# Performance work log

Measured on AMD Instinct MI355X. Metric: run time of the kernel, lower is better.

## Reference

```python
import jax, jax.numpy as jnp
import numpy as np

HIDDEN_DIM = 64
MEMORY_SLOTS = 8
SEQ_LEN = 64
VOCAB_SIZE = 64
B = 524288


def setup_inputs() -> dict:
    key = jax.random.key(0)
    k1, k2, k3, k4, k5, k6 = jax.random.split(key, 6)
    seqs = jax.random.randint(k1, (B, SEQ_LEN), 0, VOCAB_SIZE + 2, dtype=jnp.int64 if jax.config.jax_enable_x64 else jnp.int32)
    query_tok = jax.random.randint(k2, (B,), 0, VOCAB_SIZE + 2, dtype=seqs.dtype)
    embed = jax.random.normal(k3, (VOCAB_SIZE + 2, HIDDEN_DIM), dtype=jnp.float32)
    # torch Linear: y = x @ W.T + b
    W1 = jax.random.normal(k4, (HIDDEN_DIM, HIDDEN_DIM * 2), dtype=jnp.float32) * (1.0 / np.sqrt(HIDDEN_DIM * 2))
    b1 = jnp.zeros((HIDDEN_DIM,), dtype=jnp.float32)
    W2 = jax.random.normal(k5, (VOCAB_SIZE, HIDDEN_DIM), dtype=jnp.float32) * (1.0 / np.sqrt(HIDDEN_DIM))
    b2 = jnp.zeros((VOCAB_SIZE,), dtype=jnp.float32)
    return {"seqs": seqs, "query_tok": query_tok, "embed": embed,
            "W1": W1, "b1": b1, "W2": W2, "b2": b2}


def reference(seqs, query_tok, embed, W1, b1, W2, b2):
    # FIFO of capacity MEMORY_SLOTS over tokens t=0..SEQ_LEN-2 keeps exactly the
    # last MEMORY_SLOTS tokens: positions [SEQ_LEN-1-MEMORY_SLOTS, SEQ_LEN-1).
    win = seqs[:, SEQ_LEN - 1 - MEMORY_SLOTS : SEQ_LEN - 1]        # [B, 8]
    mem_summary = embed[win].mean(axis=1)                          # [B, H]
    q_emb = embed[query_tok]                                       # [B, H]
    h = jnp.concatenate([q_emb, mem_summary], axis=-1)             # [B, 2H]
    h = jax.nn.relu(h @ W1.T + b1)                                 # [B, H]
    logits = h @ W2.T + b2                                         # [B, VOCAB]
    return logits
```

## Files before the change

kernel.cpp:

```cpp
#include <hip/hip_runtime.h>

#define HID 64
#define NTOK 66
#define SEQ 64
#define WIN0 55
#define NW 8
#define LDS_STRIDE 72
#define ITERS 8
#define BLOCK 512
#define ROWS_PER_ITER 128
#define HOFF (2 * NTOK * LDS_STRIDE)
#define HBUF (ROWS_PER_ITER * LDS_STRIDE)

typedef _Float16 half8 __attribute__((ext_vector_type(8)));
typedef unsigned short ushort8v __attribute__((ext_vector_type(8)));
typedef float float4v __attribute__((ext_vector_type(4)));

static __device__ __forceinline__ unsigned short f2h(float f) {
    _Float16 h = (_Float16)f;
    union { _Float16 h; unsigned short u; } v; v.h = h;
    return v.u;
}

__global__ void build_tables(const float* __restrict__ embed,
                             const float* __restrict__ W1,
                             const float* __restrict__ b1,
                             unsigned short* __restrict__ tbl) {
    int b = blockIdx.x;
    int tb = b & 1;
    int t  = b >> 1;
    int n  = threadIdx.x;
    float acc = tb ? 0.0f : b1[n];
    const float* er = embed + t * HID;
    const float* wr = W1 + n * (2 * HID) + tb * HID;
#pragma unroll 8
    for (int k = 0; k < HID; ++k) acc += er[k] * wr[k];
    if (tb) acc *= 0.125f;
    tbl[tb * (NTOK * HID) + t * HID + n] = f2h(acc);
}

__global__ __launch_bounds__(BLOCK, 2) void fused_forward(
    const int* __restrict__ seqs,
    const int* __restrict__ qtok,
    const float* __restrict__ W2,
    const float* __restrict__ b2,
    const unsigned short* __restrict__ tbl,
    float* __restrict__ out)
{
    __shared__ unsigned short T_lds[HOFF + 2 * HBUF];

    int tid  = threadIdx.x;
    int wv   = tid >> 6;
    int l    = tid & 63;
    int lrow = l & 15;
    int lg   = l >> 4;
    int lk8  = lg * 8;
    int tile0 = wv & 3;

    int blk0 = blockIdx.x * (ITERS * ROWS_PER_ITER);
    int prow0 = blk0 + tile0 * 16 + lrow;
    int prow1 = prow0 + 64;

    int qA0, qA1, qB0, qB1;
    int wA0[NW], wA1[NW], wB0[NW], wB1[NW];

#define LOADT(S, t_) if ((t_) < ITERS) { \
    int r0_ = prow0 + (t_) * ROWS_PER_ITER; \
    int r1_ = prow1 + (t_) * ROWS_PER_ITER; \
    q##S##0 = qtok[r0_]; \
    q##S##1 = qtok[r1_]; \
    const int* s0_ = seqs + r0_ * SEQ + WIN0; \
    const int* s1_ = seqs + r1_ * SEQ + WIN0; \
    _Pragma("unroll") \
    for (int j = 0; j < NW; ++j) { w##S##0[j] = s0_[j]; w##S##1[j] = s1_[j]; } \
}

#define RD_T1(qq, koff) (*(const half8*)(T_lds + (qq) * LDS_STRIDE + (koff)))
#define RD_T2(ww, koff) (*(const half8*)(T_lds + NTOK * LDS_STRIDE + (ww) * LDS_STRIDE + (koff)))

#define PRODUCE(S, buf_) { \
    unsigned short* hb_ = T_lds + HOFF + (buf_) * HBUF; \
    half8 s0_ = RD_T1(q##S##0, lk8); \
    half8 s1_ = RD_T1(q##S##0, 32 + lk8); \
    half8 u0_ = RD_T1(q##S##1, lk8); \
    half8 u1_ = RD_T1(q##S##1, 32 + lk8); \
    _Pragma("unroll") \
    for (int j = 0; j < NW; ++j) { \
        s0_ += RD_T2(w##S##0[j], lk8); \
        s1_ += RD_T2(w##S##0[j], 32 + lk8); \
        u0_ += RD_T2(w##S##1[j], lk8); \
        u1_ += RD_T2(w##S##1[j], 32 + lk8); \
    } \
    half8 z_ = (half8)(_Float16)0; \
    s0_ = __builtin_elementwise_max(s0_, z_); \
    s1_ = __builtin_elementwise_max(s1_, z_); \
    u0_ = __builtin_elementwise_max(u0_, z_); \
    u1_ = __builtin_elementwise_max(u1_, z_); \
    unsigned short* r0_ = hb_ + (tile0 * 16 + lrow) * LDS_STRIDE; \
    unsigned short* r1_ = hb_ + ((tile0 + 4) * 16 + lrow) * LDS_STRIDE; \
    *(half8*)(r0_ + lk8) = s0_; \
    *(half8*)(r0_ + 32 + lk8) = s1_; \
    *(half8*)(r1_ + lk8) = u0_; \
    *(half8*)(r1_ + 32 + lk8) = u1_; \
}

#define CONSUME(t_, buf_) { \
    const unsigned short* hb_ = T_lds + HOFF + (buf_) * HBUF; \
    _Pragma("unroll") \
    for (int pt = 0; pt < 2; ++pt) { \
        int trow_ = (tile0 + pt * 4) * 16 + lrow; \
        half8 a0_ = *(const half8*)(hb_ + trow_ * LDS_STRIDE + lk8); \
        half8 a1_ = *(const half8*)(hb_ + trow_ * LDS_STRIDE + 32 + lk8); \
        float* op_ = out + (size_t)(blk0 + (t_) * ROWS_PER_ITER + trow_) * HID; \
        _Pragma("unroll") \
        for (int nt = 0; nt < 4; ++nt) { \
            float4v acc_ = __builtin_amdgcn_mfma_f32_16x16x32_f16(wfrag[nt][0], a0_, b2v[nt], 0, 0, 0); \
            acc_ = __builtin_amdgcn_mfma_f32_16x16x32_f16(wfrag[nt][1], a1_, acc_, 0, 0, 0); \
            *(float4v*)(op_ + nt * 16 + lg * 4) = acc_; \
        } \
    } \
}

#define ITER_E(t_) { \
    if (wv >= 4) { CONSUME(t_, (t_) & 1); } \
    else if ((t_) + 1 < ITERS) { PRODUCE(B, ((t_) + 1) & 1); LOADT(B, (t_) + 3); } \
    __syncthreads(); \
}
#define ITER_O(t_) { \
    if (wv >= 4) { CONSUME(t_, (t_) & 1); } \
    else if ((t_) + 1 < ITERS) { PRODUCE(A, ((t_) + 1) & 1); LOADT(A, (t_) + 3); } \
    __syncthreads(); \
}

    half8   wfrag[4][2];
    float4v b2v[4];
    if (wv < 4) {
        LOADT(A, 0);
        LOADT(B, 1);
    } else {
#pragma unroll
        for (int nt = 0; nt < 4; ++nt) {
            b2v[nt] = *(const float4v*)(b2 + nt * 16 + lg * 4);
#pragma unroll
            for (int kc = 0; kc < 2; ++kc) {
                const float* wp = W2 + (nt * 16 + lrow) * HID + kc * 32 + lk8;
                half8 f;
#pragma unroll
                for (int j = 0; j < 8; ++j) f[j] = (_Float16)wp[j];
                wfrag[nt][kc] = f;
            }
        }
    }

    for (int i = tid; i < 2 * NTOK * (HID / 8); i += BLOCK) {
        int tbi = i / (NTOK * 8);
        int rem = i - tbi * (NTOK * 8);
        int t   = rem >> 3;
        int kq  = (rem & 7) << 3;
        *(ushort8v*)(T_lds + tbi * (NTOK * LDS_STRIDE) + t * LDS_STRIDE + kq) =
            *(const ushort8v*)(tbl + tbi * (NTOK * HID) + t * HID + kq);
    }
    __syncthreads();

    if (wv < 4) {
        PRODUCE(A, 0);
        LOADT(A, 2);
    }
    __syncthreads();

    ITER_E(0);  ITER_O(1);  ITER_E(2);  ITER_O(3);
    ITER_E(4);  ITER_O(5);  ITER_E(6);  ITER_O(7);

#undef LOADT
#undef RD_T1
#undef RD_T2
#undef PRODUCE
#undef CONSUME
#undef ITER_E
#undef ITER_O
}

extern "C" void kernel_launch(void* const* d_in, const int* in_sizes, int n_in,
                              void* d_out, int out_size, void* d_ws, size_t ws_size,
                              hipStream_t stream) {
    const int*   seqs  = (const int*)d_in[0];
    const int*   qtok  = (const int*)d_in[1];
    const float* embed = (const float*)d_in[2];
    const float* W1    = (const float*)d_in[3];
    const float* b1    = (const float*)d_in[4];
    const float* W2    = (const float*)d_in[5];
    const float* b2    = (const float*)d_in[6];
    float* out = (float*)d_out;
    unsigned short* tbl = (unsigned short*)d_ws;

    int B = in_sizes[0] / SEQ;

    build_tables<<<NTOK * 2, HID, 0, stream>>>(embed, W1, b1, tbl);

    int grid = B / (ITERS * ROWS_PER_ITER);
    fused_forward<<<grid, BLOCK, 0, stream>>>(seqs, qtok, W2, b2, tbl, out);
}
```

Measured before the change: 46.40 us.

## Process two row-tiles per barrier with four-deep LDS ring and more rows per block

Doubles rows per block (ITERS 8 to 16) and restructures the producer/consumer pipeline so each barrier round produces and consumes two 128-row tiles, using four H buffers in LDS and four sets of prefetched token registers. The aim is to halve the number of __syncthreads per row and to deepen global prefetch so the index loads are further ahead of use. In exchange it uses more LDS and registers (four q/w register sets), which may lower occupancy, and the grid is halved.

```diff
diff --git a/kernel.cpp b/kernel.cpp
--- a/kernel.cpp
+++ b/kernel.cpp
@@ -6,7 +6,7 @@
 #define WIN0 55
 #define NW 8
 #define LDS_STRIDE 72
-#define ITERS 8
+#define ITERS 16
 #define BLOCK 512
 #define ROWS_PER_ITER 128
 #define HOFF (2 * NTOK * LDS_STRIDE)
@@ -47,7 +47,7 @@
     const unsigned short* __restrict__ tbl,
     float* __restrict__ out)
 {
-    __shared__ unsigned short T_lds[HOFF + 2 * HBUF];
+    __shared__ unsigned short T_lds[HOFF + 4 * HBUF];
 
     int tid  = threadIdx.x;
     int wv   = tid >> 6;
@@ -61,35 +61,38 @@
     int prow0 = blk0 + tile0 * 16 + lrow;
     int prow1 = prow0 + 64;
 
-    int qA0, qA1, qB0, qB1;
-    int wA0[NW], wA1[NW], wB0[NW], wB1[NW];
-
-#define LOADT(S, t_) if ((t_) < ITERS) { \
+    int qS0, qS1, qS2, qS3;
+    int wS0[NW], wS1[NW], wS2[NW], wS3[NW];
+
+#define LOADT(S, t_) { \
     int r0_ = prow0 + (t_) * ROWS_PER_ITER; \
     int r1_ = prow1 + (t_) * ROWS_PER_ITER; \
-    q##S##0 = qtok[r0_]; \
-    q##S##1 = qtok[r1_]; \
+    qS##S = qtok[r0_]; \
+     \
+    q2S##S = qtok[r1_]; \
     const int* s0_ = seqs + r0_ * SEQ + WIN0; \
     const int* s1_ = seqs + r1_ * SEQ + WIN0; \
     _Pragma("unroll") \
-    for (int j = 0; j < NW; ++j) { w##S##0[j] = s0_[j]; w##S##1[j] = s1_[j]; } \
-}
+    for (int j = 0; j < NW; ++j) { wS##S[j] = s0_[j]; w2S##S[j] = s1_[j]; } \
+}
+    int q2S0, q2S1, q2S2, q2S3;
+    int w2S0[NW], w2S1[NW], w2S2[NW], w2S3[NW];
 
 #define RD_T1(qq, koff) (*(const half8*)(T_lds + (qq) * LDS_STRIDE + (koff)))
 #define RD_T2(ww, koff) (*(const half8*)(T_lds + NTOK * LDS_STRIDE + (ww) * LDS_STRIDE + (koff)))
 
 #define PRODUCE(S, buf_) { \
     unsigned short* hb_ = T_lds + HOFF + (buf_) * HBUF; \
-    half8 s0_ = RD_T1(q##S##0, lk8); \
-    half8 s1_ = RD_T1(q##S##0, 32 + lk8); \
-    half8 u0_ = RD_T1(q##S##1, lk8); \
-    half8 u1_ = RD_T1(q##S##1, 32 + lk8); \
+    half8 s0_ = RD_T1(qS##S, lk8); \
+    half8 s1_ = RD_T1(qS##S, 32 + lk8); \
+    half8 u0_ = RD_T1(q2S##S, lk8); \
+    half8 u1_ = RD_T1(q2S##S, 32 + lk8); \
     _Pragma("unroll") \
     for (int j = 0; j < NW; ++j) { \
-        s0_ += RD_T2(w##S##0[j], lk8); \
-        s1_ += RD_T2(w##S##0[j], 32 + lk8); \
-        u0_ += RD_T2(w##S##1[j], lk8); \
-        u1_ += RD_T2(w##S##1[j], 32 + lk8); \
+        s0_ += RD_T2(wS##S[j], lk8); \
+        s1_ += RD_T2(wS##S[j], 32 + lk8); \
+        u0_ += RD_T2(w2S##S[j], lk8); \
+        u1_ += RD_T2(w2S##S[j], 32 + lk8); \
     } \
     half8 z_ = (half8)(_Float16)0; \
     s0_ = __builtin_elementwise_max(s0_, z_); \
@@ -121,22 +124,23 @@
     } \
 }
 
-#define ITER_E(t_) { \
-    if (wv >= 4) { CONSUME(t_, (t_) & 1); } \
-    else if ((t_) + 1 < ITERS) { PRODUCE(B, ((t_) + 1) & 1); LOADT(B, (t_) + 3); } \
-    __syncthreads(); \
-}
-#define ITER_O(t_) { \
-    if (wv >= 4) { CONSUME(t_, (t_) & 1); } \
-    else if ((t_) + 1 < ITERS) { PRODUCE(A, ((t_) + 1) & 1); LOADT(A, (t_) + 3); } \
+#define ROUND(i0, i1, l0, l1, doload) { \
+    if (wv >= 4) { CONSUME(i0, (i0) & 3); CONSUME(i1, (i1) & 3); } \
+    else { \
+        PRODUCE(((i0 + 2) & 3), ((i0 + 2) & 3)); \
+        PRODUCE(((i1 + 2) & 3), ((i1 + 2) & 3)); \
+        if (doload) { LOADT(((l0) & 3), l0); LOADT(((l1) & 3), l1); } \
+    } \
     __syncthreads(); \
 }
 
     half8   wfrag[4][2];
     float4v b2v[4];
     if (wv < 4) {
-        LOADT(A, 0);
-        LOADT(B, 1);
+        LOADT(0, 0);
+        LOADT(1, 1);
+        LOADT(2, 2);
+        LOADT(3, 3);
     } else {
 #pragma unroll
         for (int nt = 0; nt < 4; ++nt) {
@@ -163,21 +167,40 @@
     __syncthreads();
 
     if (wv < 4) {
-        PRODUCE(A, 0);
-        LOADT(A, 2);
+        PRODUCE(0, 0);
+        PRODUCE(1, 1);
     }
     __syncthreads();
 
-    ITER_E(0);  ITER_O(1);  ITER_E(2);  ITER_O(3);
-    ITER_E(4);  ITER_O(5);  ITER_E(6);  ITER_O(7);
+    if (wv >= 4) { CONSUME(0, 0); CONSUME(1, 1); }
+    else { PRODUCE(2, 2); PRODUCE(3, 3); LOADT(0, 4); LOADT(1, 5); }
+    __syncthreads();
+    if (wv >= 4) { CONSUME(2, 2); CONSUME(3, 3); }
+    else { PRODUCE(0, 0); PRODUCE(1, 1); LOADT(2, 6); LOADT(3, 7); }
+    __syncthreads();
+    if (wv >= 4) { CONSUME(4, 0); CONSUME(5, 1); }
+    else { PRODUCE(2, 2); PRODUCE(3, 3); LOADT(0, 8); LOADT(1, 9); }
+    __syncthreads();
+    if (wv >= 4) { CONSUME(6, 2); CONSUME(7, 3); }
+    else { PRODUCE(0, 0); PRODUCE(1, 1); LOADT(2, 10); LOADT(3, 11); }
+    __syncthreads();
+    if (wv >= 4) { CONSUME(8, 0); CONSUME(9, 1); }
+    else { PRODUCE(2, 2); PRODUCE(3, 3); LOADT(0, 12); LOADT(1, 13); }
+    __syncthreads();
+    if (wv >= 4) { CONSUME(10, 2); CONSUME(11, 3); }
+    else { PRODUCE(0, 0); PRODUCE(1, 1); LOADT(2, 14); LOADT(3, 15); }
+    __syncthreads();
+    if (wv >= 4) { CONSUME(12, 0); CONSUME(13, 1); }
+    else { PRODUCE(2, 2); PRODUCE(3, 3); }
+    __syncthreads();
+    if (wv >= 4) { CONSUME(14, 2); CONSUME(15, 3); }
 
 #undef LOADT
 #undef RD_T1
 #undef RD_T2
 #undef PRODUCE
 #undef CONSUME
-#undef ITER_E
-#undef ITER_O
+#undef ROUND
 }
 
 extern "C" void kernel_launch(void* const* d_in, const int* in_sizes, int n_in,
```

After: 47.52 us. 1.02x slower.
